# Performance work log

Hardware: AMD Instinct MI355X
Metric: run time of the kernel (lower is better)

## Reference

```python
import jax, jax.numpy as jnp
import numpy as np

B, N, C, F, E, K = 2, 2048, 1024, 4096, 8, 2

def setup_inputs() -> dict:
    key = jax.random.key(0)
    k = jax.random.split(key, 6)
    xavier1 = float(np.sqrt(6.0 / (C + F)))
    xavier2 = float(np.sqrt(6.0 / (F + C)))
    return {
        "x": jax.random.normal(k[0], (B, N, C), dtype=jnp.float32),
        "router_w": jax.random.normal(k[1], (E, C), dtype=jnp.float32) * 0.01,
        "w1": jax.random.uniform(k[2], (E, F, C), dtype=jnp.float32, minval=-xavier1, maxval=xavier1),
        "b1": jnp.zeros((E, F), dtype=jnp.float32),
        "w2": jax.random.uniform(k[3], (E, C, F), dtype=jnp.float32, minval=-xavier2, maxval=xavier2),
        "b2": jnp.zeros((E, C), dtype=jnp.float32),
    }

def reference(x, router_w, w1, b1, w2, b2):
    Bb, Nn, Cc = x.shape
    x_flat = x.reshape(-1, Cc)                                   # [T, C]
    # Router (eval mode: no noise)
    logits = jnp.einsum('tc,ec->te', x_flat, router_w)           # [T, E]
    probs = jax.nn.softmax(logits, axis=-1)
    top_w, top_idx = jax.lax.top_k(probs, K)                     # [T, K]
    top_w = top_w / (jnp.sum(top_w, axis=-1, keepdims=True) + 1e-9)
    # Dense all-expert MLP (same math as the per-expert gather/scatter loop)
    h = jnp.einsum('tc,efc->tef', x_flat, w1) + b1[None]          # [T, E, F]
    h = jax.nn.relu(h)
    y = jnp.einsum('tef,ecf->tec', h, w2) + b2[None]              # [T, E, C]
    # Gather the K selected experts per token and combine
    sel = jnp.take_along_axis(y, top_idx[:, :, None], axis=1)    # [T, K, C]
    out = jnp.einsum('tkc,tk->tc', sel, top_w)                   # [T, C]
    return out.reshape(Bb, Nn, Cc)
```

## Files before the change

kernel.cpp:

```cpp
#include <hip/hip_runtime.h>
#include <hip/hip_fp16.h>


#define T_TOK 4096
#define C_DIM 1024
#define F_DIM 4096
#define E_NUM 8
#define BM 128
#define BN 128
#define BK 64
#define MAXT 72
#define NP   (MAXT * BM)
#define TILE_H 8192

typedef float f32x4 __attribute__((ext_vector_type(4)));
typedef _Float16 half8 __attribute__((ext_vector_type(8)));

#define AS1 __attribute__((address_space(1)))
#define AS3 __attribute__((address_space(3)))

__device__ __forceinline__ int swz(int r, int ec) { return ec ^ ((r & 7) << 3); }

__device__ __forceinline__ half8 cvt8(float4 f0, float4 f1) {
  half8 hv;
  hv[0] = (_Float16)f0.x; hv[1] = (_Float16)f0.y; hv[2] = (_Float16)f0.z; hv[3] = (_Float16)f0.w;
  hv[4] = (_Float16)f1.x; hv[5] = (_Float16)f1.y; hv[6] = (_Float16)f1.z; hv[7] = (_Float16)f1.w;
  return hv;
}

__device__ __forceinline__ int xcd_swz(int bid, int nwg) {
  int xcd = bid & 7, rest = bid >> 3;
  int q = nwg >> 3, r = nwg & 7;
  return (xcd < r ? xcd * (q + 1) : r * (q + 1) + (xcd - r) * q) + rest;
}

__global__ __launch_bounds__(256) void router_kernel(
    const float* __restrict__ x, const float* __restrict__ rw,
    int* __restrict__ top_idx, float* __restrict__ top_w)
{
  int t = blockIdx.x * 4 + (threadIdx.x >> 6);
  int lane = threadIdx.x & 63;
  const float* xr = x + (size_t)t * C_DIM;
  float acc[E_NUM];
#pragma unroll
  for (int e = 0; e < E_NUM; ++e) acc[e] = 0.f;
  for (int j = 0; j < C_DIM / 64; ++j) {
    int c = j * 64 + lane;
    float xv = xr[c];
#pragma unroll
    for (int e = 0; e < E_NUM; ++e) acc[e] += xv * rw[e * C_DIM + c];
  }
#pragma unroll
  for (int e = 0; e < E_NUM; ++e) {
    float v = acc[e];
#pragma unroll
    for (int off = 32; off > 0; off >>= 1) v += __shfl_xor(v, off);
    acc[e] = v;
  }
  if (lane == 0) {
    float mx = acc[0];
    for (int e = 1; e < E_NUM; ++e) mx = fmaxf(mx, acc[e]);
    float p[E_NUM]; float Z = 0.f;
    for (int e = 0; e < E_NUM; ++e) { p[e] = expf(acc[e] - mx); Z += p[e]; }
    int b0 = 0;
    for (int e = 1; e < E_NUM; ++e) if (p[e] > p[b0]) b0 = e;
    int b1i = -1; float pb = -1.f;
    for (int e = 0; e < E_NUM; ++e) if (e != b0 && p[e] > pb) { pb = p[e]; b1i = e; }
    float p0 = p[b0] / Z, p1 = pb / Z;
    float s = p0 + p1 + 1e-9f;
    top_idx[t * 2 + 0] = b0;
    top_idx[t * 2 + 1] = b1i;
    top_w[t * 2 + 0] = p0 / s;
    top_w[t * 2 + 1] = p1 / s;
  }
}

__global__ void build_lists(const int* __restrict__ top_idx,
                            int* __restrict__ rows_g, int* __restrict__ counts,
                            int* __restrict__ tile_off, int* __restrict__ inv)
{
  int e = threadIdx.x >> 6;
  int lane = threadIdx.x & 63;
  int cnt = 0;
  for (int t0 = 0; t0 < T_TOK; t0 += 64) {
    int t = t0 + lane;
    bool sel = (top_idx[t * 2] == e) || (top_idx[t * 2 + 1] == e);
    cnt += __popcll(__ballot(sel));
  }
  if (lane == 0) counts[e] = cnt;
  __syncthreads();
  if (threadIdx.x == 0) {
    int o = 0;
    for (int i = 0; i < E_NUM; ++i) { tile_off[i] = o; o += (counts[i] + BM - 1) / BM; }
    tile_off[E_NUM] = o;
  }
  __syncthreads();
  int base = tile_off[e] * BM;
  int pos = 0;
  for (int t0 = 0; t0 < T_TOK; t0 += 64) {
    int t = t0 + lane;
    int i0 = top_idx[t * 2], i1 = top_idx[t * 2 + 1];
    bool sel = (i0 == e) || (i1 == e);
    unsigned long long mask = __ballot(sel);
    if (sel) {
      int p = pos + __popcll(mask & ((1ull << lane) - 1ull));
      int slot = t * 2 + ((i0 == e) ? 0 : 1);
      rows_g[base + p] = slot;
      inv[slot] = (e << 16) | (base + p);
    }
    pos += __popcll(mask);
  }
}

__global__ __launch_bounds__(256) void gather_x(
    const float* __restrict__ x, const int* __restrict__ rows_g,
    const int* __restrict__ counts, const int* __restrict__ tile_off,
    _Float16* __restrict__ xg)
{
  unsigned g = blockIdx.x * 256 + threadIdx.x;
  unsigned p = g >> 7, ccr = g & 127;
  int gt = p >> 7, r = p & 127;
  int kc = ccr >> 3, c8 = ccr & 7;
  int e = -1;
#pragma unroll
  for (int i = 0; i < E_NUM; ++i)
    if (gt >= tile_off[i] && gt < tile_off[i + 1]) e = i;
  half8 hv = {};
  if (e >= 0) {
    int nrem = counts[e] - (gt - tile_off[e]) * BM;
    if (r < nrem) {
      int t = rows_g[p] >> 1;
      const float4* s = reinterpret_cast<const float4*>(x + (size_t)t * C_DIM + kc * 64 + c8 * 8);
      hv = cvt8(s[0], s[1]);
    }
  }
  *reinterpret_cast<half8*>(xg + ((size_t)gt * 16 + kc) * TILE_H + r * 64 + ((c8 ^ (r & 7)) << 3)) = hv;
}

__global__ __launch_bounds__(256) void cvt_w1(
    const float* __restrict__ src, _Float16* __restrict__ dst, int ch, int Fc, int lgFc)
{
  unsigned g = blockIdx.x * 256 + threadIdx.x;
  unsigned row = g >> 7, ccr = g & 127;
  int e = row >> lgFc, frow = row & (Fc - 1);
  int ftl = frow >> 7, r = frow & 127;
  int kc = ccr >> 3, c8 = ccr & 7;
  const float4* s = reinterpret_cast<const float4*>(
      src + ((size_t)e * F_DIM + ch * Fc + frow) * C_DIM + kc * 64 + c8 * 8);
  int nft = Fc >> 7;
  size_t tix = ((size_t)(e * nft + ftl) * 16 + kc);
  *reinterpret_cast<half8*>(dst + tix * TILE_H + r * 64 + ((c8 ^ (r & 7)) << 3)) = cvt8(s[0], s[1]);
}

__global__ __launch_bounds__(256) void cvt_w2(
    const float* __restrict__ src, _Float16* __restrict__ dst, int ch, int Fc, int lgc)
{
  unsigned g = blockIdx.x * 256 + threadIdx.x;
  unsigned row = g >> lgc, ccr = g & ((Fc >> 3) - 1);
  int e = row >> 10, c = row & 1023;
  int ct = c >> 7, r = c & 127;
  int kc = ccr >> 3, c8 = ccr & 7;
  const float4* s = reinterpret_cast<const float4*>(
      src + (size_t)row * F_DIM + ch * Fc + kc * 64 + c8 * 8);
  int nkc = Fc >> 6;
  size_t tix = ((size_t)(e * 8 + ct) * nkc + kc);
  *reinterpret_cast<half8*>(dst + tix * TILE_H + r * 64 + ((c8 ^ (r & 7)) << 3)) = cvt8(s[0], s[1]);
}

#define STAGE_TILE(At_, Bt_, kc_)                                                 \
  {                                                                               \
    const _Float16* a_ = (At_) + (size_t)(kc_) * TILE_H + wave * 2048 + lane * 8; \
    const _Float16* b_ = (Bt_) + (size_t)(kc_) * TILE_H + wave * 2048 + lane * 8; \
    _Pragma("unroll")                                                             \
    for (int c_ = 0; c_ < 4; ++c_) {                                              \
      __builtin_amdgcn_global_load_lds((const AS1 void*)(a_ + c_ * 512),          \
          (AS3 void*)(&As[(wave * 4 + c_) * 512]), 16, 0, 0);                     \
      __builtin_amdgcn_global_load_lds((const AS1 void*)(b_ + c_ * 512),          \
          (AS3 void*)(&Bs[(wave * 4 + c_) * 512]), 16, 0, 0);                     \
    }                                                                             \
  }

#define COMPUTE_TILE()                                                            \
  _Pragma("unroll")                                                               \
  for (int kk = 0; kk < BK; kk += 32) {                                           \
    const int klo = kk + (lane >> 4) * 8;                                         \
    half8 aF[4], bF[4];                                                           \
    _Pragma("unroll")                                                             \
    for (int m = 0; m < 4; ++m) {                                                 \
      int r = wr * 64 + m * 16 + (lane & 15);                                     \
      aF[m] = *reinterpret_cast<const half8*>(&As[r * BK + swz(r, klo)]);         \
    }                                                                             \
    _Pragma("unroll")                                                             \
    for (int n = 0; n < 4; ++n) {                                                 \
      int r = wc * 64 + n * 16 + (lane & 15);                                     \
      bF[n] = *reinterpret_cast<const half8*>(&Bs[r * BK + swz(r, klo)]);         \
    }                                                                             \
    _Pragma("unroll")                                                             \
    for (int m = 0; m < 4; ++m)                                                   \
      _Pragma("unroll")                                                           \
      for (int n = 0; n < 4; ++n)                                                 \
        acc[m][n] = __builtin_amdgcn_mfma_f32_16x16x32_f16(aF[m], bF[n], acc[m][n], 0, 0, 0); \
  }

__global__ __launch_bounds__(256) void gemm1_kernel(
    const _Float16* __restrict__ xg, const _Float16* __restrict__ w1t,
    const float* __restrict__ b1, const int* __restrict__ counts,
    const int* __restrict__ tile_off, _Float16* __restrict__ ht,
    int ch, int Fc)
{
  const int wgid = xcd_swz(blockIdx.x, gridDim.x);
  const int ft = wgid / MAXT;
  const int gt = wgid - ft * MAXT;
  if (gt >= tile_off[E_NUM]) return;
  int e = 0;
  while (gt >= tile_off[e + 1]) ++e;
  const int nrem = min(counts[e] - (gt - tile_off[e]) * BM, BM);
  const int nft = Fc >> 7;
  const _Float16* At = xg + (size_t)gt * 16 * TILE_H;
  const _Float16* Bt = w1t + (size_t)(e * nft + ft) * 16 * TILE_H;

  __shared__ __align__(16) _Float16 As[TILE_H];
  __shared__ __align__(16) _Float16 Bs[TILE_H];

  const int tid = threadIdx.x;
  const int lane = tid & 63;
  const int wave = tid >> 6;
  const int wr = wave >> 1, wc = wave & 1;

  f32x4 acc[4][4];
#pragma unroll
  for (int m = 0; m < 4; ++m)
#pragma unroll
    for (int n = 0; n < 4; ++n) acc[m][n] = (f32x4){0.f, 0.f, 0.f, 0.f};

  for (int kc = 0; kc < 16; ++kc) {
    STAGE_TILE(At, Bt, kc);
    __syncthreads();
    COMPUTE_TILE();
    __syncthreads();
  }

  const int nkcF = Fc >> 6;
#pragma unroll
  for (int m = 0; m < 4; ++m) {
#pragma unroll
    for (int j = 0; j < 4; ++j) {
      int iloc = wr * 64 + m * 16 + (lane >> 4) * 4 + j;
      if (iloc < nrem) {
#pragma unroll
        for (int n = 0; n < 4; ++n) {
          int fl = ft * BN + wc * 64 + n * 16 + (lane & 15);
          float v = acc[m][n][j] + b1[e * F_DIM + ch * Fc + fl];
          _Float16 h = (_Float16)fmaxf(v, 0.f);
          ht[((size_t)gt * nkcF + (fl >> 6)) * TILE_H + iloc * 64 +
             ((((fl >> 3) & 7) ^ (iloc & 7)) << 3) + (fl & 7)] = h;
        }
      }
    }
  }
}

__global__ __launch_bounds__(256) void gemm2_kernel(
    const _Float16* __restrict__ ht, const _Float16* __restrict__ w2t,
    const int* __restrict__ tile_off, _Float16* __restrict__ y,
    int Fc, int kspl, int accum)
{
  const int wgid = xcd_swz(blockIdx.x, gridDim.x);
  const int ctks = wgid / MAXT;
  const int gt = wgid - ctks * MAXT;
  if (gt >= tile_off[E_NUM]) return;
  const int ct = ctks & 7;
  const int ks = ctks >> 3;
  int e = 0;
  while (gt >= tile_off[e + 1]) ++e;
  const int nkc = Fc >> 6;
  const int klen = nkc / kspl;
  const _Float16* At = ht + ((size_t)gt * nkc + ks * klen) * TILE_H;
  const _Float16* Bt = w2t + ((size_t)(e * 8 + ct) * nkc + ks * klen) * TILE_H;

  __shared__ __align__(16) _Float16 As[TILE_H];
  __shared__ __align__(16) _Float16 Bs[TILE_H];

  const int tid = threadIdx.x;
  const int lane = tid & 63;
  const int wave = tid >> 6;
  const int wr = wave >> 1, wc = wave & 1;

  f32x4 acc[4][4];
#pragma unroll
  for (int m = 0; m < 4; ++m)
#pragma unroll
    for (int n = 0; n < 4; ++n) acc[m][n] = (f32x4){0.f, 0.f, 0.f, 0.f};

  for (int kc = 0; kc < klen; ++kc) {
    STAGE_TILE(At, Bt, kc);
    __syncthreads();
    COMPUTE_TILE();
    __syncthreads();
  }

  _Float16* yk = y + ((size_t)(ks * MAXT + gt) * BM) * C_DIM;
#pragma unroll
  for (int m = 0; m < 4; ++m) {
#pragma unroll
    for (int j = 0; j < 4; ++j) {
      int iloc = wr * 64 + m * 16 + (lane >> 4) * 4 + j;
#pragma unroll
      for (int n = 0; n < 4; ++n) {
        int c = ct * BN + wc * 64 + n * 16 + (lane & 15);
        _Float16* p = yk + (size_t)iloc * C_DIM + c;
        float v = acc[m][n][j];
        if (accum) v += (float)*p;
        *p = (_Float16)v;
      }
    }
  }
}

__global__ __launch_bounds__(256) void combine_kernel(
    const _Float16* __restrict__ y, const int* __restrict__ inv,
    const float* __restrict__ top_w, const float* __restrict__ b2,
    float* __restrict__ out, int kspl)
{
  int g = blockIdx.x * 256 + threadIdx.x;
  int t = g >> 7, c8 = (g & 127) << 3;
  float o[8];
#pragma unroll
  for (int i = 0; i < 8; ++i) o[i] = 0.f;
#pragma unroll
  for (int k = 0; k < 2; ++k) {
    int iv = inv[t * 2 + k];
    int e = iv >> 16, pos = iv & 0xffff;
    float w = top_w[t * 2 + k];
    const float4* bb = reinterpret_cast<const float4*>(b2 + e * C_DIM + c8);
    float4 bv0 = bb[0], bv1 = bb[1];
    float s[8] = {bv0.x, bv0.y, bv0.z, bv0.w, bv1.x, bv1.y, bv1.z, bv1.w};
    for (int ks = 0; ks < kspl; ++ks) {
      half8 hv = *reinterpret_cast<const half8*>(
          y + ((size_t)(ks * MAXT * BM + pos)) * C_DIM + c8);
#pragma unroll
      for (int i = 0; i < 8; ++i) s[i] += (float)hv[i];
    }
#pragma unroll
    for (int i = 0; i < 8; ++i) o[i] += w * s[i];
  }
  float4* op = reinterpret_cast<float4*>(out + (size_t)t * C_DIM + c8);
  op[0] = (float4){o[0], o[1], o[2], o[3]};
  op[1] = (float4){o[4], o[5], o[6], o[7]};
}

extern "C" void kernel_launch(void* const* d_in, const int* in_sizes, int n_in,
                              void* d_out, int out_size, void* d_ws, size_t ws_size,
                              hipStream_t stream)
{
  const float* x  = (const float*)d_in[0];
  const float* rw = (const float*)d_in[1];
  const float* w1 = (const float*)d_in[2];
  const float* b1 = (const float*)d_in[3];
  const float* w2 = (const float*)d_in[4];
  const float* b2 = (const float*)d_in[5];
  float* out = (float*)d_out;

  char* ws = (char*)d_ws;
  size_t off = 0;
  auto carve = [&](size_t bytes) -> void* {
    void* p = ws + off;
    off += (bytes + 255) & ~(size_t)255;
    return p;
  };
  int*   top_idx  = (int*)carve((size_t)T_TOK * 2 * sizeof(int));
  float* top_w    = (float*)carve((size_t)T_TOK * 2 * sizeof(float));
  int*   counts   = (int*)carve(E_NUM * sizeof(int));
  int*   tile_off = (int*)carve((E_NUM + 1) * sizeof(int));
  int*   rows_g   = (int*)carve((size_t)NP * sizeof(int));
  int*   inv      = (int*)carve((size_t)T_TOK * 2 * sizeof(int));
  _Float16* xg    = (_Float16*)carve((size_t)MAXT * 16 * TILE_H * sizeof(_Float16));
  _Float16* y     = (_Float16*)carve((size_t)2 * NP * C_DIM * sizeof(_Float16));
  size_t fixed = off;

  int nchunk = 8;
  const int cands[4] = {1, 2, 4, 8};
  for (int ci = 0; ci < 4; ++ci) {
    int n = cands[ci];
    size_t fc = (size_t)(F_DIM / n);
    size_t w1b = ((size_t)E_NUM * fc * C_DIM * 2 + 255) & ~(size_t)255;
    size_t w2b = ((size_t)E_NUM * C_DIM * fc * 2 + 255) & ~(size_t)255;
    size_t htb = ((size_t)MAXT * (fc >> 6) * TILE_H * 2 + 255) & ~(size_t)255;
    if (fixed + w1b + w2b + htb <= ws_size) { nchunk = n; break; }
  }
  const int Fc = F_DIM / nchunk;
  int lgFc = 0; while ((1 << lgFc) < Fc) ++lgFc;
  _Float16* w1t = (_Float16*)carve((size_t)E_NUM * Fc * C_DIM * sizeof(_Float16));
  _Float16* w2t = (_Float16*)carve((size_t)E_NUM * C_DIM * Fc * sizeof(_Float16));
  _Float16* ht  = (_Float16*)carve((size_t)MAXT * (Fc >> 6) * TILE_H * sizeof(_Float16));

  const int kspl = (Fc >= 2048) ? 2 : 1;

  router_kernel<<<T_TOK / 4, 256, 0, stream>>>(x, rw, top_idx, top_w);
  build_lists<<<1, 512, 0, stream>>>(top_idx, rows_g, counts, tile_off, inv);
  gather_x<<<(MAXT * BM * 128) / 256, 256, 0, stream>>>(x, rows_g, counts, tile_off, xg);

  const int cvt_blocks = 4 * Fc;
  for (int ch = 0; ch < nchunk; ++ch) {
    cvt_w1<<<cvt_blocks, 256, 0, stream>>>(w1, w1t, ch, Fc, lgFc);
    cvt_w2<<<cvt_blocks, 256, 0, stream>>>(w2, w2t, ch, Fc, lgFc - 3);
    gemm1_kernel<<<MAXT * (Fc / BN), 256, 0, stream>>>(
        xg, w1t, b1, counts, tile_off, ht, ch, Fc);
    gemm2_kernel<<<MAXT * 8 * kspl, 256, 0, stream>>>(
        ht, w2t, tile_off, y, Fc, kspl, ch != 0);
  }
  combine_kernel<<<(T_TOK * 128) / 256, 256, 0, stream>>>(y, inv, top_w, b2, out, kspl);
}
```

Before: 382.0 us.

## Widen GEMM tiles to 128x256 with 8-wave blocks and grouped tile ordering

Doubles the N tile of both expert GEMMs from 128 to 256 by staging two weight tiles per k-step into shared memory, using 512-thread blocks with a 2x4 wave layout. Each token tile loaded into LDS is therefore reused across twice as many output columns, halving A-operand traffic. Block indices are also regrouped so eight consecutive token tiles share the same weight tile, for better L2 locality. The cost is 48KB of LDS per block and half as many blocks, which lowers occupancy and parallelism.

```diff
diff --git a/kernel.cpp b/kernel.cpp
--- a/kernel.cpp
+++ b/kernel.cpp
@@ -7,7 +7,7 @@
 #define F_DIM 4096
 #define E_NUM 8
 #define BM 128
-#define BN 128
+#define BN 256
 #define BK 64
 #define MAXT 72
 #define NP   (MAXT * BM)
@@ -167,16 +167,17 @@
   *reinterpret_cast<half8*>(dst + tix * TILE_H + r * 64 + ((c8 ^ (r & 7)) << 3)) = cvt8(s[0], s[1]);
 }
 
-#define STAGE_TILE(At_, Bt_, kc_)                                                 \
+#define STAGE_TILE(aSrc_, b0Src_, b1Src_)                                         \
   {                                                                               \
-    const _Float16* a_ = (At_) + (size_t)(kc_) * TILE_H + wave * 2048 + lane * 8; \
-    const _Float16* b_ = (Bt_) + (size_t)(kc_) * TILE_H + wave * 2048 + lane * 8; \
     _Pragma("unroll")                                                             \
-    for (int c_ = 0; c_ < 4; ++c_) {                                              \
-      __builtin_amdgcn_global_load_lds((const AS1 void*)(a_ + c_ * 512),          \
-          (AS3 void*)(&As[(wave * 4 + c_) * 512]), 16, 0, 0);                     \
-      __builtin_amdgcn_global_load_lds((const AS1 void*)(b_ + c_ * 512),          \
-          (AS3 void*)(&Bs[(wave * 4 + c_) * 512]), 16, 0, 0);                     \
+    for (int i_ = 0; i_ < 2; ++i_) {                                              \
+      int o_ = tid * 8 + i_ * 4096;                                               \
+      __builtin_amdgcn_global_load_lds((const AS1 void*)((aSrc_) + o_),           \
+          (AS3 void*)(&As[o_]), 16, 0, 0);                                        \
+      __builtin_amdgcn_global_load_lds((const AS1 void*)((b0Src_) + o_),          \
+          (AS3 void*)(&Bs[o_]), 16, 0, 0);                                        \
+      __builtin_amdgcn_global_load_lds((const AS1 void*)((b1Src_) + o_),          \
+          (AS3 void*)(&Bs[8192 + o_]), 16, 0, 0);                                 \
     }                                                                             \
   }
 
@@ -192,8 +193,9 @@
     }                                                                             \
     _Pragma("unroll")                                                             \
     for (int n = 0; n < 4; ++n) {                                                 \
-      int r = wc * 64 + n * 16 + (lane & 15);                                     \
-      bF[n] = *reinterpret_cast<const half8*>(&Bs[r * BK + swz(r, klo)]);         \
+      int br = wc * 64 + n * 16 + (lane & 15);                                    \
+      bF[n] = *reinterpret_cast<const half8*>(                                    \
+          &Bs[(br >> 7) * 8192 + (br & 127) * 64 + swz(br, klo)]);                \
     }                                                                             \
     _Pragma("unroll")                                                             \
     for (int m = 0; m < 4; ++m)                                                   \
@@ -202,30 +204,34 @@
         acc[m][n] = __builtin_amdgcn_mfma_f32_16x16x32_f16(aF[m], bF[n], acc[m][n], 0, 0, 0); \
   }
 
-__global__ __launch_bounds__(256) void gemm1_kernel(
+__global__ __launch_bounds__(512) void gemm1_kernel(
     const _Float16* __restrict__ xg, const _Float16* __restrict__ w1t,
     const float* __restrict__ b1, const int* __restrict__ counts,
     const int* __restrict__ tile_off, _Float16* __restrict__ ht,
     int ch, int Fc)
 {
+  const int NFT = Fc / BN;
   const int wgid = xcd_swz(blockIdx.x, gridDim.x);
-  const int ft = wgid / MAXT;
-  const int gt = wgid - ft * MAXT;
+  const int grp = wgid / (8 * NFT);
+  const int rem = wgid - grp * 8 * NFT;
+  const int ft = rem >> 3;
+  const int gt = grp * 8 + (rem & 7);
   if (gt >= tile_off[E_NUM]) return;
   int e = 0;
   while (gt >= tile_off[e + 1]) ++e;
   const int nrem = min(counts[e] - (gt - tile_off[e]) * BM, BM);
-  const int nft = Fc >> 7;
-  const _Float16* At = xg + (size_t)gt * 16 * TILE_H;
-  const _Float16* Bt = w1t + (size_t)(e * nft + ft) * 16 * TILE_H;
+  const int nftl = Fc >> 7;
+  const _Float16* At  = xg + (size_t)gt * 16 * TILE_H;
+  const _Float16* Bt0 = w1t + (size_t)(e * nftl + 2 * ft) * 16 * TILE_H;
+  const _Float16* Bt1 = w1t + (size_t)(e * nftl + 2 * ft + 1) * 16 * TILE_H;
 
   __shared__ __align__(16) _Float16 As[TILE_H];
-  __shared__ __align__(16) _Float16 Bs[TILE_H];
+  __shared__ __align__(16) _Float16 Bs[2 * TILE_H];
 
   const int tid = threadIdx.x;
   const int lane = tid & 63;
   const int wave = tid >> 6;
-  const int wr = wave >> 1, wc = wave & 1;
+  const int wr = wave >> 2, wc = wave & 3;
 
   f32x4 acc[4][4];
 #pragma unroll
@@ -234,7 +240,7 @@
     for (int n = 0; n < 4; ++n) acc[m][n] = (f32x4){0.f, 0.f, 0.f, 0.f};
 
   for (int kc = 0; kc < 16; ++kc) {
-    STAGE_TILE(At, Bt, kc);
+    STAGE_TILE(At + (size_t)kc * TILE_H, Bt0 + (size_t)kc * TILE_H, Bt1 + (size_t)kc * TILE_H);
     __syncthreads();
     COMPUTE_TILE();
     __syncthreads();
@@ -260,31 +266,35 @@
   }
 }
 
-__global__ __launch_bounds__(256) void gemm2_kernel(
+__global__ __launch_bounds__(512) void gemm2_kernel(
     const _Float16* __restrict__ ht, const _Float16* __restrict__ w2t,
     const int* __restrict__ tile_off, _Float16* __restrict__ y,
     int Fc, int kspl, int accum)
 {
+  const int NCMB = 4 * kspl;
   const int wgid = xcd_swz(blockIdx.x, gridDim.x);
-  const int ctks = wgid / MAXT;
-  const int gt = wgid - ctks * MAXT;
+  const int grp = wgid / (8 * NCMB);
+  const int rem = wgid - grp * 8 * NCMB;
+  const int cmb = rem >> 3;
+  const int gt = grp * 8 + (rem & 7);
   if (gt >= tile_off[E_NUM]) return;
-  const int ct = ctks & 7;
-  const int ks = ctks >> 3;
+  const int ct = cmb & 3;
+  const int ks = cmb >> 2;
   int e = 0;
   while (gt >= tile_off[e + 1]) ++e;
   const int nkc = Fc >> 6;
   const int klen = nkc / kspl;
-  const _Float16* At = ht + ((size_t)gt * nkc + ks * klen) * TILE_H;
-  const _Float16* Bt = w2t + ((size_t)(e * 8 + ct) * nkc + ks * klen) * TILE_H;
+  const _Float16* At  = ht + ((size_t)gt * nkc + ks * klen) * TILE_H;
+  const _Float16* Bt0 = w2t + ((size_t)(e * 8 + 2 * ct) * nkc + ks * klen) * TILE_H;
+  const _Float16* Bt1 = w2t + ((size_t)(e * 8 + 2 * ct + 1) * nkc + ks * klen) * TILE_H;
 
   __shared__ __align__(16) _Float16 As[TILE_H];
-  __shared__ __align__(16) _Float16 Bs[TILE_H];
+  __shared__ __align__(16) _Float16 Bs[2 * TILE_H];
 
   const int tid = threadIdx.x;
   const int lane = tid & 63;
   const int wave = tid >> 6;
-  const int wr = wave >> 1, wc = wave & 1;
+  const int wr = wave >> 2, wc = wave & 3;
 
   f32x4 acc[4][4];
 #pragma unroll
@@ -293,7 +303,7 @@
     for (int n = 0; n < 4; ++n) acc[m][n] = (f32x4){0.f, 0.f, 0.f, 0.f};
 
   for (int kc = 0; kc < klen; ++kc) {
-    STAGE_TILE(At, Bt, kc);
+    STAGE_TILE(At + (size_t)kc * TILE_H, Bt0 + (size_t)kc * TILE_H, Bt1 + (size_t)kc * TILE_H);
     __syncthreads();
     COMPUTE_TILE();
     __syncthreads();
@@ -404,9 +414,9 @@
   for (int ch = 0; ch < nchunk; ++ch) {
     cvt_w1<<<cvt_blocks, 256, 0, stream>>>(w1, w1t, ch, Fc, lgFc);
     cvt_w2<<<cvt_blocks, 256, 0, stream>>>(w2, w2t, ch, Fc, lgFc - 3);
-    gemm1_kernel<<<MAXT * (Fc / BN), 256, 0, stream>>>(
+    gemm1_kernel<<<MAXT * (Fc / BN), 512, 0, stream>>>(
         xg, w1t, b1, counts, tile_off, ht, ch, Fc);
-    gemm2_kernel<<<MAXT * 8 * kspl, 256, 0, stream>>>(
+    gemm2_kernel<<<MAXT * 4 * kspl, 512, 0, stream>>>(
         ht, w2t, tile_off, y, Fc, kspl, ch != 0);
   }
   combine_kernel<<<(T_TOK * 128) / 256, 256, 0, stream>>>(y, inv, top_w, b2, out, kspl);
```

Result: faster. 355.2 us (-7.0%).
